# Kernel optimization log

Measured on AMD Instinct MI355X. Metric: run time of the kernel, lower is better.

## Reference

```python
import jax, jax.numpy as jnp
import numpy as np

N_NODES = 50000
N_EDGES = 200000
D = 384
R = 2  # num_relations


def setup_inputs() -> dict:
    key = jax.random.key(0)
    ks = jax.random.split(key, 16)
    inp = {
        "embeddings": jax.random.normal(ks[0], (N_NODES, D), dtype=jnp.float32),
        "edge_index": jax.random.randint(ks[1], (2, N_EDGES), 0, N_NODES, dtype=jnp.int64),
        "edge_type": jax.random.randint(ks[2], (N_EDGES,), 0, R, dtype=jnp.int64),
    }
    # RGCNConv params for 3 layers: per-relation weight, root weight, bias
    s = 1.0 / np.sqrt(D)
    for i, kk in zip((1, 2, 3), range(3)):
        inp[f"W{i}"] = jax.random.uniform(ks[3 + 3 * kk], (R, D, D), dtype=jnp.float32, minval=-s, maxval=s)
        inp[f"root{i}"] = jax.random.uniform(ks[4 + 3 * kk], (D, D), dtype=jnp.float32, minval=-s, maxval=s)
        inp[f"bias{i}"] = jnp.zeros((D,), dtype=jnp.float32)
    return inp


def _rgcn_conv(x, src, dst, edge_type, W, root, bias):
    # PyG RGCNConv with aggr='mean': for each relation, mean-aggregate neighbor
    # features over edges of that relation, then apply relation weight; plus
    # root transform and bias. We transform-then-aggregate (equivalent, linear).
    out = x @ root + bias
    for r in range(R):
        xr = x @ W[r]                                   # [N, D]
        mask = (edge_type == r).astype(x.dtype)         # [E]
        msg = xr[src] * mask[:, None]                   # [E, D] gather
        s = jax.ops.segment_sum(msg, dst, num_segments=N_NODES)    # [N, D]
        cnt = jax.ops.segment_sum(mask, dst, num_segments=N_NODES)  # [N]
        out = out + s / jnp.maximum(cnt, 1.0)[:, None]  # mean (0 if no edges)
    return out


def reference(embeddings, edge_index, edge_type, W1, root1, bias1, W2, root2, bias2, W3, root3, bias3):
    src, dst = edge_index[0], edge_index[1]
    x = jax.nn.relu(_rgcn_conv(embeddings, src, dst, edge_type, W1, root1, bias1))
    # dropout is identity in eval mode
    x = jax.nn.relu(_rgcn_conv(x, src, dst, edge_type, W2, root2, bias2))
    x = _rgcn_conv(x, src, dst, edge_type, W3, root3, bias3)
    return x
```

## Files before the change

### kernel.cpp

```cpp
#include <hip/hip_runtime.h>
#include <hip/hip_bf16.h>


#define D 384
#define NC 1152
#define BM 256
#define BN 128
#define BK 32
#define NKT (D / BK)
#define NTN (NC / BN)

typedef __attribute__((ext_vector_type(8))) short short8;
typedef __attribute__((ext_vector_type(4))) float floatx4;
typedef unsigned int uint;
typedef unsigned short ushort;

#define BAR() asm volatile("s_barrier" ::: "memory")
#define WAIT_VM3() asm volatile("s_waitcnt vmcnt(3)" ::: "memory")
#define WAIT_VM0() asm volatile("s_waitcnt vmcnt(0)" ::: "memory")

__device__ __forceinline__ void load_lds16(const void* g, void* l) {
    __builtin_amdgcn_global_load_lds(
        (const __attribute__((address_space(1))) void*)g,
        (__attribute__((address_space(3))) void*)l, 16, 0, 0);
}

__device__ __forceinline__ ushort f2bf(float x) {
    __hip_bfloat16 h = __float2bfloat16(x);
    return *reinterpret_cast<ushort*>(&h);
}

__device__ __forceinline__ uint pack2(float a, float b) {
    return (uint)f2bf(a) | ((uint)f2bf(b) << 16);
}

__device__ __forceinline__ void stage_a(const ushort* __restrict__ g,
                                        ushort* l, int grow0, int kt,
                                        int rmax, int tid)
{
#pragma unroll
    for (int j = 0; j < 2; ++j) {
        const int ch = j * 512 + tid;
        const int row = ch >> 2;
        const int cs = ch & 3;
        const int gc = cs ^ ((row >> 1) & 3);
        const int gr = min(grow0 + row, rmax);
        load_lds16(g + (size_t)gr * D + kt * BK + gc * 8, l + (size_t)ch * 8);
    }
}

__device__ __forceinline__ void stage_b(const ushort* __restrict__ g,
                                        ushort* l, int grow0, int kt, int tid)
{
    const int row = tid >> 2;
    const int cs = tid & 3;
    const int gc = cs ^ ((row >> 1) & 3);
    load_lds16(g + (size_t)(grow0 + row) * D + kt * BK + gc * 8,
               l + (size_t)tid * 8);
}

__global__ __launch_bounds__(512, 4) void gemm_bf16_mfma(
    const ushort* __restrict__ A, const ushort* __restrict__ BT,
    ushort* __restrict__ C, int M, int nwg)
{
    __shared__ alignas(16) ushort As[3][BM * BK];
    __shared__ alignas(16) ushort Bs[3][BN * BK];

    const int o = blockIdx.x;
    const int xcd = o & 7, lid = o >> 3;
    const int q = nwg >> 3, r = nwg & 7;
    const int wg = (xcd < r ? xcd * (q + 1) : r * (q + 1) + (xcd - r) * q) + lid;
    const int bnt = wg % NTN, bmt = wg / NTN;
    const int bm = bmt * BM, bn = bnt * BN;

    const int tid = threadIdx.x;
    const int wave = tid >> 6, lane = tid & 63;
    const int wm = wave >> 1;
    const int wn = wave & 1;
    const int l15 = lane & 15, k8 = lane >> 4;

    floatx4 acc[4][4] = {};

    stage_a(A, As[0], bm, 0, M - 1, tid);
    stage_b(BT, Bs[0], bn, 0, tid);
    stage_a(A, As[1], bm, 1, M - 1, tid);
    stage_b(BT, Bs[1], bn, 1, tid);
    WAIT_VM3();
    BAR();

    for (int j = 0; j < NKT; ++j) {
        const ushort* Ab = As[j % 3];
        const ushort* Bb = Bs[j % 3];

        short8 af[4], bf[4];
#pragma unroll
        for (int nf = 0; nf < 4; ++nf) {
            const int rr = wn * 64 + nf * 16 + l15;
            af[nf] = *(const short8*)(Bb + rr * BK + ((k8 ^ ((rr >> 1) & 3)) << 3));
        }
#pragma unroll
        for (int mf = 0; mf < 4; ++mf) {
            const int rr = wm * 64 + mf * 16 + l15;
            bf[mf] = *(const short8*)(Ab + rr * BK + ((k8 ^ ((rr >> 1) & 3)) << 3));
        }

        const int js = j + 2;
        if (js < NKT) {
            stage_a(A, As[js % 3], bm, js, M - 1, tid);
            stage_b(BT, Bs[js % 3], bn, js, tid);
        }

        __builtin_amdgcn_s_setprio(1);
#pragma unroll
        for (int nf = 0; nf < 4; ++nf)
#pragma unroll
            for (int mf = 0; mf < 4; ++mf)
                acc[nf][mf] = __builtin_amdgcn_mfma_f32_16x16x32_bf16(
                    af[nf], bf[mf], acc[nf][mf], 0, 0, 0);
        __builtin_amdgcn_s_setprio(0);

        if (j <= NKT - 3)      { WAIT_VM3(); }
        else if (j == NKT - 2) { WAIT_VM0(); }
        BAR();
    }

    const int node0 = bm + wm * 64 + l15;
    const int col0 = bn + wn * 64 + k8 * 4;
    if (bm + BM <= M) {
#pragma unroll
        for (int mf = 0; mf < 4; ++mf) {
            uint2* rowp = (uint2*)(C + (size_t)(node0 + mf * 16) * NC + col0);
#pragma unroll
            for (int nf = 0; nf < 4; ++nf) {
                uint2 o2;
                o2.x = pack2(acc[nf][mf][0], acc[nf][mf][1]);
                o2.y = pack2(acc[nf][mf][2], acc[nf][mf][3]);
                rowp[nf * 4] = o2;
            }
        }
    } else {
#pragma unroll
        for (int mf = 0; mf < 4; ++mf) {
            const int node = node0 + mf * 16;
            if (node < M) {
                uint2* rowp = (uint2*)(C + (size_t)node * NC + col0);
#pragma unroll
                for (int nf = 0; nf < 4; ++nf) {
                    uint2 o2;
                    o2.x = pack2(acc[nf][mf][0], acc[nf][mf][1]);
                    o2.y = pack2(acc[nf][mf][2], acc[nf][mf][3]);
                    rowp[nf * 4] = o2;
                }
            }
        }
    }
}


__global__ __launch_bounds__(256) void count_edges(
    const int* __restrict__ dst, const int* __restrict__ et,
    int* __restrict__ cntI, int E, int M)
{
    const int e = blockIdx.x * blockDim.x + threadIdx.x;
    if (e < E) atomicAdd(&cntI[(size_t)et[e] * M + dst[e]], 1);
}

__global__ __launch_bounds__(256) void finalize_cnt(
    const int* __restrict__ cntI, float* __restrict__ invc, int n)
{
    const int i = blockIdx.x * blockDim.x + threadIdx.x;
    if (i < n) invc[i] = 1.0f / (float)max(cntI[i], 1);
}

__global__ __launch_bounds__(1024) void scan_local(
    const int* __restrict__ hist, int* __restrict__ offs,
    int* __restrict__ bsums, int n)
{
    __shared__ int tmp[1024];
    const int tid = threadIdx.x;
    const int i = blockIdx.x * 1024 + tid;
    const int v = (i < n) ? hist[i] : 0;
    tmp[tid] = v;
    __syncthreads();
#pragma unroll
    for (int off = 1; off < 1024; off <<= 1) {
        const int add = (tid >= off) ? tmp[tid - off] : 0;
        __syncthreads();
        tmp[tid] += add;
        __syncthreads();
    }
    if (i < n) offs[i] = tmp[tid] - v;
    if (tid == 1023) bsums[blockIdx.x] = tmp[1023];
}

__global__ __launch_bounds__(1024) void scan_bsums(
    int* __restrict__ bsums, int* __restrict__ total_out, int nb)
{
    __shared__ int tmp[1024];
    const int tid = threadIdx.x;
    const int v = (tid < nb) ? bsums[tid] : 0;
    tmp[tid] = v;
    __syncthreads();
#pragma unroll
    for (int off = 1; off < 1024; off <<= 1) {
        const int add = (tid >= off) ? tmp[tid - off] : 0;
        __syncthreads();
        tmp[tid] += add;
        __syncthreads();
    }
    if (tid < nb) bsums[tid] = tmp[tid] - v;
    if (tid == 1023) *total_out = tmp[1023];
}

__global__ __launch_bounds__(1024) void scan_add(
    int* __restrict__ offs, const int* __restrict__ bsums, int n)
{
    const int i = blockIdx.x * 1024 + threadIdx.x;
    if (i < n) offs[i] += bsums[blockIdx.x];
}

__global__ __launch_bounds__(256) void fill_sorted(
    const int* __restrict__ src, const int* __restrict__ dst,
    const int* __restrict__ et, const int* __restrict__ offs,
    int* __restrict__ cursor, int* __restrict__ sorted, int E, int M)
{
    const int e = blockIdx.x * blockDim.x + threadIdx.x;
    if (e < E) {
        const int key = et[e] * M + dst[e];
        const int pos = offs[key] + atomicAdd(&cursor[key], 1);
        sorted[pos] = src[e];
    }
}

__global__ __launch_bounds__(256) void build_bt(
    const float* __restrict__ root1, const float* __restrict__ W1,
    const float* __restrict__ root2, const float* __restrict__ W2,
    const float* __restrict__ root3, const float* __restrict__ W3,
    ushort* __restrict__ BT)
{
    __shared__ float tile[32][33];
    const int l = blockIdx.z;
    const float* root = (l == 0) ? root1 : (l == 1) ? root2 : root3;
    const float* W    = (l == 0) ? W1    : (l == 1) ? W2    : W3;
    const int kt = blockIdx.x * 32;
    const int nt = blockIdx.y * 32;
    const int tx = threadIdx.x & 31;
    const int ty = threadIdx.x >> 5;
    const float* srcm;
    int noff;
    if (nt < D)          { srcm = root;      noff = 0; }
    else if (nt < 2 * D) { srcm = W;         noff = D; }
    else                 { srcm = W + D * D; noff = 2 * D; }
    const int n = nt - noff + tx;
#pragma unroll
    for (int i = 0; i < 4; ++i) {
        const int k = kt + ty + i * 8;
        tile[ty + i * 8][tx] = srcm[(size_t)k * D + n];
    }
    __syncthreads();
    ushort* dst = BT + (size_t)l * NC * D;
#pragma unroll
    for (int i = 0; i < 4; ++i) {
        const int nn = nt + ty + i * 8;
        const int kk = kt + tx;
        dst[(size_t)nn * D + kk] = f2bf(tile[tx][ty + i * 8]);
    }
}

__global__ __launch_bounds__(256) void cast_f32_to_bf16(
    const float* __restrict__ x, ushort* __restrict__ y, int n4)
{
    const int i = blockIdx.x * blockDim.x + threadIdx.x;
    if (i < n4) {
        const float4 v = ((const float4*)x)[i];
        uint2 o;
        o.x = pack2(v.x, v.y);
        o.y = pack2(v.z, v.w);
        ((uint2*)y)[i] = o;
    }
}

__global__ __launch_bounds__(256) void aggregate_all(
    const ushort* __restrict__ TC, const int* __restrict__ sorted,
    const int* __restrict__ offs, const float* __restrict__ invc,
    const float* __restrict__ bias, ushort* __restrict__ outb,
    float* __restrict__ outf, int M, int relu)
{
    const int wave = threadIdx.x >> 6;
    const int lane = threadIdx.x & 63;
    const int d = blockIdx.x * 4 + wave;
    if (d >= M) return;

    float v[6];
    {
        const uint* rp = (const uint*)(TC + (size_t)d * NC);
#pragma unroll
        for (int p = 0; p < 3; ++p) {
            const uint b = rp[lane + 64 * p];
            const float2 bb = *(const float2*)(bias + (lane + 64 * p) * 2);
            v[2 * p]     = __uint_as_float(b << 16) + bb.x;
            v[2 * p + 1] = __uint_as_float(b & 0xffff0000u) + bb.y;
        }
    }
#pragma unroll
    for (int r = 0; r < 2; ++r) {
        const int key = r * M + d;
        const int beg = offs[key], end = offs[key + 1];
        float g[6] = {0.f, 0.f, 0.f, 0.f, 0.f, 0.f};
        for (int i = beg; i < end; ++i) {
            const int s = sorted[i];
            const uint* tp = (const uint*)(TC + (size_t)s * NC + D + r * D);
#pragma unroll
            for (int p = 0; p < 3; ++p) {
                const uint b = tp[lane + 64 * p];
                g[2 * p]     += __uint_as_float(b << 16);
                g[2 * p + 1] += __uint_as_float(b & 0xffff0000u);
            }
        }
        const float ic = invc[key];
#pragma unroll
        for (int j = 0; j < 6; ++j) v[j] += ic * g[j];
    }
    if (relu) {
#pragma unroll
        for (int j = 0; j < 6; ++j) v[j] = fmaxf(v[j], 0.f);
    }
    if (outb) {
        uint* op = (uint*)(outb + (size_t)d * D);
#pragma unroll
        for (int p = 0; p < 3; ++p) op[lane + 64 * p] = pack2(v[2 * p], v[2 * p + 1]);
    } else {
        float2* op = (float2*)(outf + (size_t)d * D);
#pragma unroll
        for (int p = 0; p < 3; ++p)
            op[lane + 64 * p] = make_float2(v[2 * p], v[2 * p + 1]);
    }
}

extern "C" void kernel_launch(void* const* d_in, const int* in_sizes, int n_in,
                              void* d_out, int out_size, void* d_ws, size_t ws_size,
                              hipStream_t stream)
{
    const float* emb   = (const float*)d_in[0];
    const int*   eidx  = (const int*)d_in[1];
    const int*   et    = (const int*)d_in[2];
    const float* W1    = (const float*)d_in[3];
    const float* root1 = (const float*)d_in[4];
    const float* bias1 = (const float*)d_in[5];
    const float* W2    = (const float*)d_in[6];
    const float* root2 = (const float*)d_in[7];
    const float* bias2 = (const float*)d_in[8];
    const float* W3    = (const float*)d_in[9];
    const float* root3 = (const float*)d_in[10];
    const float* bias3 = (const float*)d_in[11];

    float* out = (float*)d_out;
    const int M = in_sizes[0] / D;
    const int E = in_sizes[1] / 2;
    const int* src  = eidx;
    const int* dstv = eidx + E;

    const int n = 2 * M;
    const int nb = (n + 1023) / 1024;

    char* w = (char*)d_ws;
    ushort* TC = (ushort*)w;          w += (size_t)M * NC * 2;
    ushort* Xb = (ushort*)w;          w += (size_t)M * D * 2;
    ushort* BT = (ushort*)w;          w += (size_t)3 * NC * D * 2;
    float* invcnt = (float*)w;        w += (size_t)n * 4;
    int* cntI = (int*)w;              w += (size_t)n * 4;
    int* offs = (int*)w;              w += ((size_t)n + 1) * 4;
    int* sorted = (int*)w;            w += (size_t)E * 4;
    int* bsums = (int*)w;

    hipMemsetAsync(cntI, 0, (size_t)n * sizeof(int), stream);
    count_edges<<<(E + 255) / 256, 256, 0, stream>>>(dstv, et, cntI, E, M);
    finalize_cnt<<<(n + 255) / 256, 256, 0, stream>>>(cntI, invcnt, n);
    scan_local<<<nb, 1024, 0, stream>>>(cntI, offs, bsums, n);
    scan_bsums<<<1, 1024, 0, stream>>>(bsums, offs + n, nb);
    scan_add<<<nb, 1024, 0, stream>>>(offs, bsums, n);
    hipMemsetAsync(cntI, 0, (size_t)n * sizeof(int), stream);
    fill_sorted<<<(E + 255) / 256, 256, 0, stream>>>(src, dstv, et, offs, cntI, sorted, E, M);

    build_bt<<<dim3(D / 32, NC / 32, 3), 256, 0, stream>>>(root1, W1, root2, W2, root3, W3, BT);
    cast_f32_to_bf16<<<(M * D / 4 + 255) / 256, 256, 0, stream>>>(emb, Xb, M * D / 4);

    const int Mtiles = (M + BM - 1) / BM;
    const int nwg = Mtiles * NTN;
    const float* biases[3] = {bias1, bias2, bias3};
    for (int l = 0; l < 3; ++l) {
        gemm_bf16_mfma<<<nwg, 512, 0, stream>>>(Xb, BT + (size_t)l * NC * D, TC, M, nwg);
        const bool last = (l == 2);
        aggregate_all<<<(M + 3) / 4, 256, 0, stream>>>(
            TC, sorted, offs, invcnt, biases[l],
            last ? nullptr : Xb, last ? out : nullptr, M, last ? 0 : 1);
    }
}
```

Baseline: 510.5 us.

## Aggregate-then-transform with K-concatenated GEMM fusing bias, relu and output

Reorders each RGCN layer to mean-aggregate raw node features per relation first, then run one GEMM over the concatenated [x | agg_r0 | agg_r1] with K=1152 and N=384. Bias, relu and the bf16/fp32 output are folded into the GEMM epilogue. This removes the large M×1152 intermediate write and the gather of wide transformed rows, so the gather reads 384-wide rows instead. In exchange it adds an M×768 aggregate buffer, and the GEMM tile changes to 128x128 with 256 threads and a longer K loop.

Result: faster. 487.1 us (-4.6%).

```diff
diff --git a/kernel.cpp b/kernel.cpp
--- a/kernel.cpp
+++ b/kernel.cpp
@@ -3,12 +3,12 @@
 
 
 #define D 384
-#define NC 1152
-#define BM 256
+#define KC 1152
+#define BM 128
 #define BN 128
 #define BK 32
-#define NKT (D / BK)
-#define NTN (NC / BN)
+#define NKT (KC / BK)
+#define NTN (D / BN)
 
 typedef __attribute__((ext_vector_type(8))) short short8;
 typedef __attribute__((ext_vector_type(4))) float floatx4;
@@ -16,7 +16,7 @@
 typedef unsigned short ushort;
 
 #define BAR() asm volatile("s_barrier" ::: "memory")
-#define WAIT_VM3() asm volatile("s_waitcnt vmcnt(3)" ::: "memory")
+#define WAIT_VM4() asm volatile("s_waitcnt vmcnt(4)" ::: "memory")
 #define WAIT_VM0() asm volatile("s_waitcnt vmcnt(0)" ::: "memory")
 
 __device__ __forceinline__ void load_lds16(const void* g, void* l) {
@@ -34,34 +34,27 @@
     return (uint)f2bf(a) | ((uint)f2bf(b) << 16);
 }
 
-__device__ __forceinline__ void stage_a(const ushort* __restrict__ g,
-                                        ushort* l, int grow0, int kt,
-                                        int rmax, int tid)
+__device__ __forceinline__ void stage_rows(const ushort* __restrict__ g,
+                                           size_t stride, int koff,
+                                           ushort* l, int grow0, int rmax,
+                                           int tid)
 {
 #pragma unroll
     for (int j = 0; j < 2; ++j) {
-        const int ch = j * 512 + tid;
+        const int ch = j * 256 + tid;
         const int row = ch >> 2;
         const int cs = ch & 3;
         const int gc = cs ^ ((row >> 1) & 3);
         const int gr = min(grow0 + row, rmax);
-        load_lds16(g + (size_t)gr * D + kt * BK + gc * 8, l + (size_t)ch * 8);
-    }
-}
-
-__device__ __forceinline__ void stage_b(const ushort* __restrict__ g,
-                                        ushort* l, int grow0, int kt, int tid)
-{
-    const int row = tid >> 2;
-    const int cs = tid & 3;
-    const int gc = cs ^ ((row >> 1) & 3);
-    load_lds16(g + (size_t)(grow0 + row) * D + kt * BK + gc * 8,
-               l + (size_t)tid * 8);
-}
-
-__global__ __launch_bounds__(512, 4) void gemm_bf16_mfma(
-    const ushort* __restrict__ A, const ushort* __restrict__ BT,
-    ushort* __restrict__ C, int M, int nwg)
+        load_lds16(g + (size_t)gr * stride + koff + gc * 8, l + (size_t)ch * 8);
+    }
+}
+
+__global__ __launch_bounds__(256, 3) void gemm_fused(
+    const ushort* __restrict__ X, const ushort* __restrict__ AG,
+    const ushort* __restrict__ BT, const float* __restrict__ bias,
+    ushort* __restrict__ Xn, float* __restrict__ outf,
+    int M, int nwg, int relu)
 {
     __shared__ alignas(16) ushort As[3][BM * BK];
     __shared__ alignas(16) ushort Bs[3][BN * BK];
@@ -81,11 +74,16 @@
 
     floatx4 acc[4][4] = {};
 
-    stage_a(A, As[0], bm, 0, M - 1, tid);
-    stage_b(BT, Bs[0], bn, 0, tid);
-    stage_a(A, As[1], bm, 1, M - 1, tid);
-    stage_b(BT, Bs[1], bn, 1, tid);
-    WAIT_VM3();
+    auto stage_a = [&](int kt, ushort* dst) {
+        if (kt < 12) stage_rows(X, 384, kt * BK, dst, bm, M - 1, tid);
+        else         stage_rows(AG, 768, (kt - 12) * BK, dst, bm, M - 1, tid);
+    };
+
+    stage_a(0, As[0]);
+    stage_rows(BT, KC, 0, Bs[0], bn, D - 1, tid);
+    stage_a(1, As[1]);
+    stage_rows(BT, KC, BK, Bs[1], bn, D - 1, tid);
+    WAIT_VM4();
     BAR();
 
     for (int j = 0; j < NKT; ++j) {
@@ -106,8 +104,8 @@
 
         const int js = j + 2;
         if (js < NKT) {
-            stage_a(A, As[js % 3], bm, js, M - 1, tid);
-            stage_b(BT, Bs[js % 3], bn, js, tid);
+            stage_a(js, As[js % 3]);
+            stage_rows(BT, KC, js * BK, Bs[js % 3], bn, D - 1, tid);
         }
 
         __builtin_amdgcn_s_setprio(1);
@@ -119,38 +117,49 @@
                     af[nf], bf[mf], acc[nf][mf], 0, 0, 0);
         __builtin_amdgcn_s_setprio(0);
 
-        if (j <= NKT - 3)      { WAIT_VM3(); }
+        if (j <= NKT - 3)      { WAIT_VM4(); }
         else if (j == NKT - 2) { WAIT_VM0(); }
         BAR();
     }
 
     const int node0 = bm + wm * 64 + l15;
-    const int col0 = bn + wn * 64 + k8 * 4;
-    if (bm + BM <= M) {
-#pragma unroll
-        for (int mf = 0; mf < 4; ++mf) {
-            uint2* rowp = (uint2*)(C + (size_t)(node0 + mf * 16) * NC + col0);
+    const int colg = bn + wn * 64 + k8 * 4;
+    float4 bv[4];
+#pragma unroll
+    for (int nf = 0; nf < 4; ++nf)
+        bv[nf] = *(const float4*)(bias + colg + nf * 16);
+
+#pragma unroll
+    for (int mf = 0; mf < 4; ++mf) {
+        const int node = node0 + mf * 16;
+        if (node < M) {
+            float v[4][4];
 #pragma unroll
             for (int nf = 0; nf < 4; ++nf) {
-                uint2 o2;
-                o2.x = pack2(acc[nf][mf][0], acc[nf][mf][1]);
-                o2.y = pack2(acc[nf][mf][2], acc[nf][mf][3]);
-                rowp[nf * 4] = o2;
+                v[nf][0] = acc[nf][mf][0] + bv[nf].x;
+                v[nf][1] = acc[nf][mf][1] + bv[nf].y;
+                v[nf][2] = acc[nf][mf][2] + bv[nf].z;
+                v[nf][3] = acc[nf][mf][3] + bv[nf].w;
+                if (relu) {
+#pragma unroll
+                    for (int t = 0; t < 4; ++t) v[nf][t] = fmaxf(v[nf][t], 0.f);
+                }
             }
-        }
-    } else {
-#pragma unroll
-        for (int mf = 0; mf < 4; ++mf) {
-            const int node = node0 + mf * 16;
-            if (node < M) {
-                uint2* rowp = (uint2*)(C + (size_t)node * NC + col0);
+            if (Xn) {
+                uint2* rowp = (uint2*)(Xn + (size_t)node * D + colg);
 #pragma unroll
                 for (int nf = 0; nf < 4; ++nf) {
                     uint2 o2;
-                    o2.x = pack2(acc[nf][mf][0], acc[nf][mf][1]);
-                    o2.y = pack2(acc[nf][mf][2], acc[nf][mf][3]);
+                    o2.x = pack2(v[nf][0], v[nf][1]);
+                    o2.y = pack2(v[nf][2], v[nf][3]);
                     rowp[nf * 4] = o2;
                 }
+            } else {
+                float4* rowp = (float4*)(outf + (size_t)node * D + colg);
+#pragma unroll
+                for (int nf = 0; nf < 4; ++nf)
+                    rowp[nf * 4] = make_float4(v[nf][0], v[nf][1],
+                                               v[nf][2], v[nf][3]);
             }
         }
     }
@@ -242,28 +251,27 @@
     const int l = blockIdx.z;
     const float* root = (l == 0) ? root1 : (l == 1) ? root2 : root3;
     const float* W    = (l == 0) ? W1    : (l == 1) ? W2    : W3;
-    const int kt = blockIdx.x * 32;
-    const int nt = blockIdx.y * 32;
+    const int k0 = blockIdx.x * 32;
+    const int n0 = blockIdx.y * 32;
     const int tx = threadIdx.x & 31;
     const int ty = threadIdx.x >> 5;
     const float* srcm;
-    int noff;
-    if (nt < D)          { srcm = root;      noff = 0; }
-    else if (nt < 2 * D) { srcm = W;         noff = D; }
-    else                 { srcm = W + D * D; noff = 2 * D; }
-    const int n = nt - noff + tx;
+    int koff;
+    if (k0 < D)          { srcm = root;      koff = 0; }
+    else if (k0 < 2 * D) { srcm = W;         koff = D; }
+    else                 { srcm = W + D * D; koff = 2 * D; }
 #pragma unroll
     for (int i = 0; i < 4; ++i) {
-        const int k = kt + ty + i * 8;
-        tile[ty + i * 8][tx] = srcm[(size_t)k * D + n];
+        const int k = k0 - koff + ty + i * 8;
+        tile[ty + i * 8][tx] = srcm[(size_t)k * D + n0 + tx];
     }
     __syncthreads();
-    ushort* dst = BT + (size_t)l * NC * D;
+    ushort* dst = BT + (size_t)l * D * KC;
 #pragma unroll
     for (int i = 0; i < 4; ++i) {
-        const int nn = nt + ty + i * 8;
-        const int kk = kt + tx;
-        dst[(size_t)nn * D + kk] = f2bf(tile[tx][ty + i * 8]);
+        const int nn = n0 + ty + i * 8;
+        const int kk = k0 + tx;
+        dst[(size_t)nn * KC + kk] = f2bf(tile[tx][ty + i * 8]);
     }
 }
 
@@ -280,28 +288,16 @@
     }
 }
 
-__global__ __launch_bounds__(256) void aggregate_all(
-    const ushort* __restrict__ TC, const int* __restrict__ sorted,
+__global__ __launch_bounds__(256) void aggregate_rel(
+    const ushort* __restrict__ X, const int* __restrict__ sorted,
     const int* __restrict__ offs, const float* __restrict__ invc,
-    const float* __restrict__ bias, ushort* __restrict__ outb,
-    float* __restrict__ outf, int M, int relu)
+    ushort* __restrict__ AG, int M)
 {
     const int wave = threadIdx.x >> 6;
     const int lane = threadIdx.x & 63;
     const int d = blockIdx.x * 4 + wave;
     if (d >= M) return;
 
-    float v[6];
-    {
-        const uint* rp = (const uint*)(TC + (size_t)d * NC);
-#pragma unroll
-        for (int p = 0; p < 3; ++p) {
-            const uint b = rp[lane + 64 * p];
-            const float2 bb = *(const float2*)(bias + (lane + 64 * p) * 2);
-            v[2 * p]     = __uint_as_float(b << 16) + bb.x;
-            v[2 * p + 1] = __uint_as_float(b & 0xffff0000u) + bb.y;
-        }
-    }
 #pragma unroll
     for (int r = 0; r < 2; ++r) {
         const int key = r * M + d;
@@ -309,7 +305,7 @@
         float g[6] = {0.f, 0.f, 0.f, 0.f, 0.f, 0.f};
         for (int i = beg; i < end; ++i) {
             const int s = sorted[i];
-            const uint* tp = (const uint*)(TC + (size_t)s * NC + D + r * D);
+            const uint* tp = (const uint*)(X + (size_t)s * D);
 #pragma unroll
             for (int p = 0; p < 3; ++p) {
                 const uint b = tp[lane + 64 * p];
@@ -318,22 +314,10 @@
             }
         }
         const float ic = invc[key];
-#pragma unroll
-        for (int j = 0; j < 6; ++j) v[j] += ic * g[j];
-    }
-    if (relu) {
-#pragma unroll
-        for (int j = 0; j < 6; ++j) v[j] = fmaxf(v[j], 0.f);
-    }
-    if (outb) {
-        uint* op = (uint*)(outb + (size_t)d * D);
-#pragma unroll
-        for (int p = 0; p < 3; ++p) op[lane + 64 * p] = pack2(v[2 * p], v[2 * p + 1]);
-    } else {
-        float2* op = (float2*)(outf + (size_t)d * D);
+        uint* op = (uint*)(AG + (size_t)d * (2 * D) + r * D);
 #pragma unroll
         for (int p = 0; p < 3; ++p)
-            op[lane + 64 * p] = make_float2(v[2 * p], v[2 * p + 1]);
+            op[lane + 64 * p] = pack2(ic * g[2 * p], ic * g[2 * p + 1]);
     }
 }
 
@@ -364,9 +348,10 @@
     const int nb = (n + 1023) / 1024;
 
     char* w = (char*)d_ws;
-    ushort* TC = (ushort*)w;          w += (size_t)M * NC * 2;
-    ushort* Xb = (ushort*)w;          w += (size_t)M * D * 2;
-    ushort* BT = (ushort*)w;          w += (size_t)3 * NC * D * 2;
+    ushort* Xa  = (ushort*)w;         w += (size_t)M * D * 2;
+    ushort* Xb2 = (ushort*)w;         w += (size_t)M * D * 2;
+    ushort* AG  = (ushort*)w;         w += (size_t)M * 2 * D * 2;
+    ushort* BT  = (ushort*)w;         w += (size_t)3 * D * KC * 2;
     float* invcnt = (float*)w;        w += (size_t)n * 4;
     int* cntI = (int*)w;              w += (size_t)n * 4;
     int* offs = (int*)w;              w += ((size_t)n + 1) * 4;
@@ -382,17 +367,17 @@
     hipMemsetAsync(cntI, 0, (size_t)n * sizeof(int), stream);
     fill_sorted<<<(E + 255) / 256, 256, 0, stream>>>(src, dstv, et, offs, cntI, sorted, E, M);
 
-    build_bt<<<dim3(D / 32, NC / 32, 3), 256, 0, stream>>>(root1, W1, root2, W2, root3, W3, BT);
-    cast_f32_to_bf16<<<(M * D / 4 + 255) / 256, 256, 0, stream>>>(emb, Xb, M * D / 4);
+    build_bt<<<dim3(KC / 32, D / 32, 3), 256, 0, stream>>>(root1, W1, root2, W2, root3, W3, BT);
+    cast_f32_to_bf16<<<(M * D / 4 + 255) / 256, 256, 0, stream>>>(emb, Xa, M * D / 4);
 
     const int Mtiles = (M + BM - 1) / BM;
     const int nwg = Mtiles * NTN;
-    const float* biases[3] = {bias1, bias2, bias3};
-    for (int l = 0; l < 3; ++l) {
-        gemm_bf16_mfma<<<nwg, 512, 0, stream>>>(Xb, BT + (size_t)l * NC * D, TC, M, nwg);
-        const bool last = (l == 2);
-        aggregate_all<<<(M + 3) / 4, 256, 0, stream>>>(
-            TC, sorted, offs, invcnt, biases[l],
-            last ? nullptr : Xb, last ? out : nullptr, M, last ? 0 : 1);
-    }
-}
+    const int agg_blocks = (M + 3) / 4;
+
+    aggregate_rel<<<agg_blocks, 256, 0, stream>>>(Xa, sorted, offs, invcnt, AG, M);
+    gemm_fused<<<nwg, 256, 0, stream>>>(Xa, AG, BT, bias1, Xb2, nullptr, M, nwg, 1);
+    aggregate_rel<<<agg_blocks, 256, 0, stream>>>(Xb2, sorted, offs, invcnt, AG, M);
+    gemm_fused<<<nwg, 256, 0, stream>>>(Xb2, AG, BT + (size_t)D * KC, bias2, Xa, nullptr, M, nwg, 1);
+    aggregate_rel<<<agg_blocks, 256, 0, stream>>>(Xa, sorted, offs, invcnt, AG, M);
+    gemm_fused<<<nwg, 256, 0, stream>>>(Xa, AG, BT + (size_t)2 * D * KC, bias3, nullptr, out, M, nwg, 0);
+}
```
